# Optimization experiments

Hardware: AMD Instinct MI355X
Metric: run time of the kernel (lower is better)

The kernel has to match this reference:

```python
import math
import jax, jax.numpy as jnp
import numpy as np

SHAPES = [(80, 80), (40, 40), (20, 20), (10, 10)]
BS, LQ, D, NH, NL, NP = 8, 1000, 256, 8, 4, 4
C = D // NH


def _offset_bias():
    # replicates _reset_parameters grid_init bias for sampling_offsets
    thetas = np.arange(NH, dtype=np.float32) * (2.0 * math.pi / NH)
    grid = np.stack([np.cos(thetas), np.sin(thetas)], -1)  # [NH,2]
    grid = grid / np.abs(grid).max(-1, keepdims=True)
    grid = np.tile(grid[:, None, None, :], (1, NL, NP, 1))  # [NH,NL,NP,2]
    for i in range(NP):
        grid[:, :, i, :] *= i + 1
    return jnp.asarray(grid.reshape(-1))


def setup_inputs() -> dict:
    key = jax.random.key(0)
    ks = jax.random.split(key, 8)
    len_v = sum(h * w for h, w in SHAPES)
    s = 1.0 / math.sqrt(D)
    starts = np.cumsum([0] + [h * w for h, w in SHAPES])[:-1]
    return {
        "query": jax.random.normal(ks[0], (BS, LQ, D), jnp.float32),
        "reference_points": jax.random.uniform(ks[1], (BS, LQ, NL, 2), jnp.float32),
        "value": jax.random.normal(ks[2], (BS, len_v, D), jnp.float32),
        "w_off": jax.random.normal(ks[3], (D, NH * NL * NP * 2), jnp.float32) * 0.01,
        "b_off": _offset_bias(),
        "w_attn": jax.random.normal(ks[4], (D, NH * NL * NP), jnp.float32) * 0.01,
        "b_attn": jnp.zeros((NH * NL * NP,), jnp.float32),
        "w_v": jax.random.normal(ks[5], (D, D), jnp.float32) * s,
        "b_v": jnp.zeros((D,), jnp.float32),
        "w_o": jax.random.normal(ks[6], (D, D), jnp.float32) * s,
        "b_o": jnp.zeros((D,), jnp.float32),
        "value_spatial_shapes": jnp.array(SHAPES, jnp.int32),
        "value_level_start_index": jnp.array(starts, jnp.int32),
    }


def _sample(img, grid, H, W):
    # bilinear grid_sample, padding_mode='zeros', align_corners=False
    # img: [B, C, H*W], grid: [B, Q, P, 2] in [-1, 1] -> out [B, C, Q, P]
    x = (grid[..., 0] + 1.0) * (W * 0.5) - 0.5
    y = (grid[..., 1] + 1.0) * (H * 0.5) - 0.5
    x0 = jnp.floor(x)
    y0 = jnp.floor(y)
    fx = x - x0
    fy = y - y0
    x0i = x0.astype(jnp.int32)
    y0i = y0.astype(jnp.int32)

    def gather(xi, yi, w):
        valid = (xi >= 0) & (xi < W) & (yi >= 0) & (yi < H)
        idx = jnp.clip(yi, 0, H - 1) * W + jnp.clip(xi, 0, W - 1)
        B, Q, P = idx.shape
        g = jax.vmap(lambda im, ix: im[:, ix])(img, idx.reshape(B, Q * P))  # [B,C,QP]
        return g.reshape(B, -1, Q, P) * (w * valid)[:, None]

    return (gather(x0i, y0i, (1 - fx) * (1 - fy))
            + gather(x0i + 1, y0i, fx * (1 - fy))
            + gather(x0i, y0i + 1, (1 - fx) * fy)
            + gather(x0i + 1, y0i + 1, fx * fy))


def _forward(query, reference_points, value, w_off, b_off, w_attn, b_attn,
             w_v, b_v, w_o, b_o, shapes):
    bs, lq, _ = query.shape
    v = (value @ w_v + b_v).reshape(bs, -1, NH, C)  # [bs, len_v, NH, C]
    off = (query @ w_off + b_off).reshape(bs, lq, NH, NL, NP, 2)
    attn = jax.nn.softmax((query @ w_attn + b_attn).reshape(bs, lq, NH, NL * NP), axis=-1)
    attn = attn.reshape(bs, lq, NH, NL, NP)
    # offset normalizer is spatial_shapes flipped -> (W, H) per level
    norm = jnp.array([[w, h] for h, w in shapes], dtype=query.dtype)  # [NL,2]
    loc = reference_points[:, :, None, :, None, :] + off / norm[None, None, None, :, None, :]
    grids = 2.0 * loc - 1.0  # [bs,lq,NH,NL,NP,2]
    start = 0
    sampled = []
    for lvl, (H, W) in enumerate(shapes):
        v_l = v[:, start:start + H * W].transpose(0, 2, 3, 1).reshape(bs * NH, C, H * W)
        g_l = grids[:, :, :, lvl].transpose(0, 2, 1, 3, 4).reshape(bs * NH, lq, NP, 2)
        sampled.append(_sample(v_l, g_l, H, W))  # [bs*NH, C, lq, NP]
        start += H * W
    samp = jnp.stack(sampled, axis=3).reshape(bs * NH, C, lq, NL * NP)
    aw = attn.transpose(0, 2, 1, 3, 4).reshape(bs * NH, 1, lq, NL * NP)
    out = (samp * aw).sum(-1).reshape(bs, NH * C, lq).transpose(0, 2, 1)  # [bs,lq,D]
    return out @ w_o + b_o


def reference(query, reference_points, value, w_off, b_off, w_attn, b_attn,
              w_v, b_v, w_o, b_o, value_spatial_shapes, value_level_start_index):
    shapes = [tuple(int(x) for x in r) for r in np.asarray(value_spatial_shapes)]
    return _forward(query, reference_points, value, w_off, b_off, w_attn, b_attn,
                    w_v, b_v, w_o, b_o, shapes)
```

## Files before the change

kernel.cpp:

```cpp
#include <hip/hip_runtime.h>
#include <hip/hip_bf16.h>
#include <math.h>

#define BS     8
#define LQ     1000
#define DMODEL 256
#define NH     8
#define NLV    4
#define NPT    4
#define LEN_V  8500
#define NQ     (BS*LQ)
#define MV     (BS*LEN_V)
#define KS     8

typedef __attribute__((ext_vector_type(8))) short short8;
typedef __attribute__((ext_vector_type(4))) float floatx4;

static __device__ __forceinline__ unsigned short f2bf(float f) {
    __hip_bfloat16 h = __float2bfloat16(f);
    return __builtin_bit_cast(unsigned short, h);
}
static __device__ __forceinline__ float asf(unsigned int u) {
    return __builtin_bit_cast(float, u);
}

template <bool A_BF16, bool OUT_BF16>
__global__ __launch_bounds__(256, 2) void mfma_gemm_db(
    const void* __restrict__ Aptr, const unsigned short* __restrict__ Bfrag,
    const float* __restrict__ bias1, const float* __restrict__ bias2, int nsplit,
    void* __restrict__ Cptr, int M)
{
    __shared__ unsigned short As[2][16384];

    const int tid = threadIdx.x;
    const int l   = tid & 63;
    const int w   = tid >> 6;
    const int bn  = blockIdx.y;
    const int lm  = l & 15;
    const int lk  = l >> 4;
    const int x7  = lm & 7;
    const int N   = (int)gridDim.y * 128;
    const int n_mtiles = (M + 63) >> 6;

    short8 Bf[2][KS];
    const int u0 = bn * 8 + w * 2;
    #pragma unroll
    for (int j = 0; j < 2; ++j)
        #pragma unroll
        for (int s = 0; s < KS; ++s)
            Bf[j][s] = *(const short8*)(Bfrag + ((size_t)((u0 + j) * KS + s) * 64 + l) * 8);

    const unsigned short* Ab = (const unsigned short*)Aptr;
    const float*          Af = (const float*)Aptr;

    float4 holdf[16];
    short8 holdb[8];

    auto prefetch = [&](int tile) {
        if (A_BF16) {
            #pragma unroll
            for (int j = 0; j < 8; ++j) {
                const int vi  = j * 256 + tid;
                const int row = vi >> 5, g = vi & 31;
                int grow = tile * 64 + row; grow = grow < M ? grow : M - 1;
                holdb[j] = *(const short8*)(Ab + (size_t)grow * 256 + g * 8);
            }
        } else {
            #pragma unroll
            for (int j = 0; j < 16; ++j) {
                const int vi  = j * 256 + tid;
                const int row = vi >> 6, c4 = vi & 63;
                int grow = tile * 64 + row; grow = grow < M ? grow : M - 1;
                holdf[j] = *(const float4*)(Af + (size_t)grow * 256 + c4 * 4);
            }
        }
    };

    int bm  = blockIdx.x;
    int buf = 0;
    prefetch(bm);

    while (bm < n_mtiles) {
        const int bm_next = bm + (int)gridDim.x;

        if (A_BF16) {
            #pragma unroll
            for (int j = 0; j < 8; ++j) {
                const int vi  = j * 256 + tid;
                const int row = vi >> 5, g = vi & 31;
                const int phys = g ^ (row & 7);
                *(short8*)(&As[buf][row * 256 + phys * 8]) = holdb[j];
            }
        } else {
            #pragma unroll
            for (int j = 0; j < 16; ++j) {
                const int vi  = j * 256 + tid;
                const int row = vi >> 6, c4 = vi & 63;
                const int g = c4 >> 1, half = c4 & 1;
                const int phys = g ^ (row & 7);
                float4 f = holdf[j];
                ushort4 h;
                h.x = f2bf(f.x); h.y = f2bf(f.y); h.z = f2bf(f.z); h.w = f2bf(f.w);
                *(ushort4*)(&As[buf][row * 256 + phys * 8 + half * 4]) = h;
            }
        }
        __syncthreads();

        if (bm_next < n_mtiles) prefetch(bm_next);

        floatx4 acc[4][2];
        #pragma unroll
        for (int i = 0; i < 4; ++i)
            #pragma unroll
            for (int j = 0; j < 2; ++j)
                #pragma unroll
                for (int r = 0; r < 4; ++r) acc[i][j][r] = 0.f;

        #pragma unroll
        for (int s = 0; s < KS; ++s) {
            short8 afr[4];
            #pragma unroll
            for (int i = 0; i < 4; ++i)
                afr[i] = *(const short8*)(
                    &As[buf][(i * 16 + lm) * 256 + (((s * 4 + lk) ^ x7)) * 8]);
            #pragma unroll
            for (int i = 0; i < 4; ++i)
                #pragma unroll
                for (int j = 0; j < 2; ++j)
                    acc[i][j] = __builtin_amdgcn_mfma_f32_16x16x32_bf16(
                                    afr[i], Bf[j][s], acc[i][j], 0, 0, 0);
        }

        #pragma unroll
        for (int j = 0; j < 2; ++j) {
            const int col = bn * 128 + w * 32 + j * 16 + lm;
            const float bv = (bias2 != nullptr && col >= nsplit) ? bias2[col - nsplit]
                                                                 : bias1[col];
            #pragma unroll
            for (int i = 0; i < 4; ++i) {
                const int rbase = bm * 64 + i * 16 + lk * 4;
                #pragma unroll
                for (int r = 0; r < 4; ++r) {
                    const int row = rbase + r;
                    if (row < M) {
                        const float v = acc[i][j][r] + bv;
                        if (OUT_BF16)
                            ((unsigned short*)Cptr)[(size_t)row * N + col] = f2bf(v);
                        else
                            ((float*)Cptr)[(size_t)row * N + col] = v;
                    }
                }
            }
        }

        buf ^= 1;
        bm = bm_next;
    }
}

__global__ __launch_bounds__(256) void wtransform(
    const float* __restrict__ w_v, const float* __restrict__ w_off,
    const float* __restrict__ w_attn, const float* __restrict__ w_o,
    unsigned short* __restrict__ wv_f, unsigned short* __restrict__ woa_f,
    unsigned short* __restrict__ wo_f)
{
    const int gid = blockIdx.x * 256 + threadIdx.x;
    int chunk, mode;
    if (gid < 8192)               { chunk = gid;         mode = 0; }
    else if (gid < 8192 + 12288)  { chunk = gid - 8192;  mode = 1; }
    else                          { chunk = gid - 20480; mode = 2; }
    const int l = chunk & 63, s = (chunk >> 6) & 7, u = chunk >> 9;
    short8 o;
    #pragma unroll
    for (int j = 0; j < 8; ++j) {
        const int k = s * 32 + (l >> 4) * 8 + j;
        const int n = u * 16 + (l & 15);
        float v;
        if (mode == 0)      v = w_v[k * 256 + n];
        else if (mode == 1) v = (n < 256) ? w_off[k * 256 + n] : w_attn[k * 128 + (n - 256)];
        else                v = w_o[k * 256 + n];
        o[j] = (short)f2bf(v);
    }
    unsigned short* dp = (mode == 0 ? wv_f : mode == 1 ? woa_f : wo_f)
                         + ((size_t)(u * 8 + s) * 64 + l) * 8;
    *(short8*)dp = o;
}

__global__ __launch_bounds__(256) void ms_sample(
    const unsigned short* __restrict__ v,
    const float* __restrict__ offattn,
    const float* __restrict__ refp,
    unsigned short* __restrict__ out_pre)
{
    __shared__ float offx_s[8][16][8];
    __shared__ float offy_s[8][16][8];
    __shared__ float atw_s [8][16][8];
    __shared__ float ref_s [8][8];

    const int tid = threadIdx.x;
    const int iq0 = blockIdx.x * 8;

    if (tid < 64) {
        const int q = tid >> 3, h = tid & 7;
        const float* rowp = offattn + (size_t)(iq0 + q) * 384;
        float lg[16];
        float m = -1e30f;
        #pragma unroll
        for (int i = 0; i < 16; ++i) { lg[i] = rowp[256 + h * 16 + i]; m = fmaxf(m, lg[i]); }
        float s = 0.f;
        #pragma unroll
        for (int i = 0; i < 16; ++i) { lg[i] = __expf(lg[i] - m); s += lg[i]; }
        const float inv = 1.f / s;
        #pragma unroll
        for (int i = 0; i < 16; ++i) atw_s[q][i][h] = lg[i] * inv;
        #pragma unroll
        for (int i = 0; i < 16; ++i) {
            offx_s[q][i][h] = rowp[(h * 16 + i) * 2 + 0];
            offy_s[q][i][h] = rowp[(h * 16 + i) * 2 + 1];
        }
        if (h == 0) {
            #pragma unroll
            for (int i = 0; i < 8; ++i) ref_s[q][i] = refp[(size_t)(iq0 + q) * 8 + i];
        }
    }
    __syncthreads();

    const int q8  = tid >> 5;
    const int sub = tid & 31;
    const int h   = sub >> 2;
    const int oct = sub & 3;
    const int iq  = iq0 + q8;
    const int b   = iq / LQ;

    float acc[8] = {0.f, 0.f, 0.f, 0.f, 0.f, 0.f, 0.f, 0.f};
    const unsigned short* vb = v + (size_t)b * LEN_V * 256 + h * 32 + oct * 8;
    const int Hs[4] = {80, 40, 20, 10};
    const int st[4] = {0, 6400, 8000, 8400};

    #pragma unroll
    for (int lvl = 0; lvl < NLV; ++lvl) {
        const int W = Hs[lvl];
        const float bx = ref_s[q8][lvl * 2 + 0] * (float)W - 0.5f;
        const float by = ref_s[q8][lvl * 2 + 1] * (float)W - 0.5f;
        const unsigned short* vl = vb + (size_t)st[lvl] * 256;
        #pragma unroll
        for (int p = 0; p < NPT; ++p) {
            const int lp = lvl * 4 + p;
            const float x  = bx + offx_s[q8][lp][h];
            const float y  = by + offy_s[q8][lp][h];
            const float at = atw_s[q8][lp][h];
            const float x0f = floorf(x), y0f = floorf(y);
            const float fx = x - x0f, fy = y - y0f;
            const int x0 = (int)x0f, y0 = (int)y0f;
            const int x1 = x0 + 1,   y1 = y0 + 1;
            const int cx0 = min(max(x0, 0), W - 1);
            const int cx1 = min(max(x1, 0), W - 1);
            const int cy0 = min(max(y0, 0), W - 1);
            const int cy1 = min(max(y1, 0), W - 1);
            const float vx0 = (x0 >= 0 && x0 < W) ? 1.f : 0.f;
            const float vx1 = (x1 >= 0 && x1 < W) ? 1.f : 0.f;
            const float vy0 = (y0 >= 0 && y0 < W) ? 1.f : 0.f;
            const float vy1 = (y1 >= 0 && y1 < W) ? 1.f : 0.f;
            const float w00 = at * (1.f - fx) * (1.f - fy) * vx0 * vy0;
            const float w01 = at * fx * (1.f - fy) * vx1 * vy0;
            const float w10 = at * (1.f - fx) * fy * vx0 * vy1;
            const float w11 = at * fx * fy * vx1 * vy1;
            const unsigned short* r0 = vl + (size_t)(cy0 * W) * 256;
            const unsigned short* r1 = vl + (size_t)(cy1 * W) * 256;
            const uint4 d00 = *(const uint4*)(r0 + (size_t)cx0 * 256);
            const uint4 d01 = *(const uint4*)(r0 + (size_t)cx1 * 256);
            const uint4 d10 = *(const uint4*)(r1 + (size_t)cx0 * 256);
            const uint4 d11 = *(const uint4*)(r1 + (size_t)cx1 * 256);
            acc[0] += w00 * asf(d00.x << 16) + w01 * asf(d01.x << 16)
                    + w10 * asf(d10.x << 16) + w11 * asf(d11.x << 16);
            acc[1] += w00 * asf(d00.x & 0xffff0000u) + w01 * asf(d01.x & 0xffff0000u)
                    + w10 * asf(d10.x & 0xffff0000u) + w11 * asf(d11.x & 0xffff0000u);
            acc[2] += w00 * asf(d00.y << 16) + w01 * asf(d01.y << 16)
                    + w10 * asf(d10.y << 16) + w11 * asf(d11.y << 16);
            acc[3] += w00 * asf(d00.y & 0xffff0000u) + w01 * asf(d01.y & 0xffff0000u)
                    + w10 * asf(d10.y & 0xffff0000u) + w11 * asf(d11.y & 0xffff0000u);
            acc[4] += w00 * asf(d00.z << 16) + w01 * asf(d01.z << 16)
                    + w10 * asf(d10.z << 16) + w11 * asf(d11.z << 16);
            acc[5] += w00 * asf(d00.z & 0xffff0000u) + w01 * asf(d01.z & 0xffff0000u)
                    + w10 * asf(d10.z & 0xffff0000u) + w11 * asf(d11.z & 0xffff0000u);
            acc[6] += w00 * asf(d00.w << 16) + w01 * asf(d01.w << 16)
                    + w10 * asf(d10.w << 16) + w11 * asf(d11.w << 16);
            acc[7] += w00 * asf(d00.w & 0xffff0000u) + w01 * asf(d01.w & 0xffff0000u)
                    + w10 * asf(d10.w & 0xffff0000u) + w11 * asf(d11.w & 0xffff0000u);
        }
    }

    short8 o;
    #pragma unroll
    for (int j = 0; j < 8; ++j) o[j] = (short)f2bf(acc[j]);
    *(short8*)(out_pre + (size_t)iq * 256 + sub * 8) = o;
}

extern "C" void kernel_launch(void* const* d_in, const int* in_sizes, int n_in,
                              void* d_out, int out_size, void* d_ws, size_t ws_size,
                              hipStream_t stream)
{
    const float* query  = (const float*)d_in[0];
    const float* refp   = (const float*)d_in[1];
    const float* value  = (const float*)d_in[2];
    const float* w_off  = (const float*)d_in[3];
    const float* b_off  = (const float*)d_in[4];
    const float* w_attn = (const float*)d_in[5];
    const float* b_attn = (const float*)d_in[6];
    const float* w_v    = (const float*)d_in[7];
    const float* b_v    = (const float*)d_in[8];
    const float* w_o    = (const float*)d_in[9];
    const float* b_o    = (const float*)d_in[10];
    (void)d_in[11]; (void)d_in[12];

    float* out = (float*)d_out;

    char* ws = (char*)d_ws;
    unsigned short* v_proj  = (unsigned short*)ws;
    float*          offattn = (float*)(ws + 34816000);
    unsigned short* outpre  = (unsigned short*)(ws + 47104000);
    unsigned short* wv_f    = (unsigned short*)(ws + 51200000);
    unsigned short* woa_f   = (unsigned short*)(ws + 51331072);
    unsigned short* wo_f    = (unsigned short*)(ws + 51527680);

    dim3 blk(256);

    hipLaunchKernelGGL(wtransform, dim3(112), blk, 0, stream,
                       w_v, w_off, w_attn, w_o, wv_f, woa_f, wo_f);
    hipLaunchKernelGGL((mfma_gemm_db<false, true>), dim3(256, 2), blk, 0, stream,
                       value, wv_f, b_v, nullptr, 1 << 30, v_proj, MV);
    hipLaunchKernelGGL((mfma_gemm_db<false, false>), dim3(63, 3), blk, 0, stream,
                       query, woa_f, b_off, b_attn, 256, offattn, NQ);
    hipLaunchKernelGGL(ms_sample, dim3(1000), blk, 0, stream,
                       v_proj, offattn, refp, outpre);
    hipLaunchKernelGGL((mfma_gemm_db<true, false>), dim3(63, 2), blk, 0, stream,
                       outpre, wo_f, b_o, nullptr, 1 << 30, out, NQ);
}
```

Measured before the change: 214.3 us.

## Pre-cast inputs to bf16, DMA-load GEMM tiles, fuse output projection into sampler

```diff
diff --git a/kernel.cpp b/kernel.cpp
--- a/kernel.cpp
+++ b/kernel.cpp
@@ -24,9 +24,16 @@
     return __builtin_bit_cast(float, u);
 }
 
-template <bool A_BF16, bool OUT_BF16>
-__global__ __launch_bounds__(256, 2) void mfma_gemm_db(
-    const void* __restrict__ Aptr, const unsigned short* __restrict__ Bfrag,
+static __device__ __forceinline__ void dma16(const unsigned short* g, unsigned short* lds) {
+    __builtin_amdgcn_global_load_lds(
+        (const __attribute__((address_space(1))) unsigned int*)g,
+        (__attribute__((address_space(3))) unsigned int*)lds,
+        16, 0, 0);
+}
+
+template <bool OUT_BF16>
+__global__ __launch_bounds__(256, 2) void mfma_gemm_dma(
+    const unsigned short* __restrict__ Ab, const unsigned short* __restrict__ Bfrag,
     const float* __restrict__ bias1, const float* __restrict__ bias2, int nsplit,
     void* __restrict__ Cptr, int M)
 {
@@ -50,63 +57,29 @@
         for (int s = 0; s < KS; ++s)
             Bf[j][s] = *(const short8*)(Bfrag + ((size_t)((u0 + j) * KS + s) * 64 + l) * 8);
 
-    const unsigned short* Ab = (const unsigned short*)Aptr;
-    const float*          Af = (const float*)Aptr;
-
-    float4 holdf[16];
-    short8 holdb[8];
-
-    auto prefetch = [&](int tile) {
-        if (A_BF16) {
-            #pragma unroll
-            for (int j = 0; j < 8; ++j) {
-                const int vi  = j * 256 + tid;
-                const int row = vi >> 5, g = vi & 31;
-                int grow = tile * 64 + row; grow = grow < M ? grow : M - 1;
-                holdb[j] = *(const short8*)(Ab + (size_t)grow * 256 + g * 8);
-            }
-        } else {
-            #pragma unroll
-            for (int j = 0; j < 16; ++j) {
-                const int vi  = j * 256 + tid;
-                const int row = vi >> 6, c4 = vi & 63;
-                int grow = tile * 64 + row; grow = grow < M ? grow : M - 1;
-                holdf[j] = *(const float4*)(Af + (size_t)grow * 256 + c4 * 4);
-            }
+    auto dma_tile = [&](int tile, int buf) {
+        #pragma unroll
+        for (int j = 0; j < 8; ++j) {
+            const int slot = j * 256 + tid;
+            const int row  = slot >> 5;
+            const int gp   = slot & 31;
+            const int gc   = gp ^ (row & 7);
+            int grow = tile * 64 + row; grow = grow < M ? grow : M - 1;
+            dma16(Ab + (size_t)grow * 256 + gc * 8,
+                  &As[buf][(j * 256 + w * 64) * 8]);
         }
     };
 
     int bm  = blockIdx.x;
     int buf = 0;
-    prefetch(bm);
+    if (bm < n_mtiles) dma_tile(bm, 0);
 
     while (bm < n_mtiles) {
         const int bm_next = bm + (int)gridDim.x;
 
-        if (A_BF16) {
-            #pragma unroll
-            for (int j = 0; j < 8; ++j) {
-                const int vi  = j * 256 + tid;
-                const int row = vi >> 5, g = vi & 31;
-                const int phys = g ^ (row & 7);
-                *(short8*)(&As[buf][row * 256 + phys * 8]) = holdb[j];
-            }
-        } else {
-            #pragma unroll
-            for (int j = 0; j < 16; ++j) {
-                const int vi  = j * 256 + tid;
-                const int row = vi >> 6, c4 = vi & 63;
-                const int g = c4 >> 1, half = c4 & 1;
-                const int phys = g ^ (row & 7);
-                float4 f = holdf[j];
-                ushort4 h;
-                h.x = f2bf(f.x); h.y = f2bf(f.y); h.z = f2bf(f.z); h.w = f2bf(f.w);
-                *(ushort4*)(&As[buf][row * 256 + phys * 8 + half * 4]) = h;
-            }
-        }
+        __builtin_amdgcn_s_waitcnt(0);
         __syncthreads();
-
-        if (bm_next < n_mtiles) prefetch(bm_next);
+        if (bm_next < n_mtiles) dma_tile(bm_next, buf ^ 1);
 
         floatx4 acc[4][2];
         #pragma unroll
@@ -186,19 +159,35 @@
     *(short8*)dp = o;
 }
 
-__global__ __launch_bounds__(256) void ms_sample(
+__global__ __launch_bounds__(256) void cast2_bf16(const float* __restrict__ value,
+                                                  const float* __restrict__ query,
+                                                  unsigned short* __restrict__ out)
+{
+    const int i = blockIdx.x * 256 + threadIdx.x;
+    const float4 v = (i < 4352000) ? ((const float4*)value)[i]
+                                   : ((const float4*)query)[i - 4352000];
+    ushort4 o;
+    o.x = f2bf(v.x); o.y = f2bf(v.y); o.z = f2bf(v.z); o.w = f2bf(v.w);
+    ((ushort4*)out)[i] = o;
+}
+
+__global__ __launch_bounds__(256) void ms_sample_fused(
     const unsigned short* __restrict__ v,
     const float* __restrict__ offattn,
     const float* __restrict__ refp,
-    unsigned short* __restrict__ out_pre)
+    const unsigned short* __restrict__ wo_f,
+    const float* __restrict__ b_o,
+    float* __restrict__ out)
 {
     __shared__ float offx_s[8][16][8];
     __shared__ float offy_s[8][16][8];
     __shared__ float atw_s [8][16][8];
     __shared__ float ref_s [8][8];
+    __shared__ unsigned short P[8][256];
 
     const int tid = threadIdx.x;
-    const int iq0 = blockIdx.x * 8;
+    const int bswz = blockIdx.x & 7;
+    const int iq0  = bswz * 1000 + (blockIdx.x >> 3) * 8;
 
     if (tid < 64) {
         const int q = tid >> 3, h = tid & 7;
@@ -229,11 +218,9 @@
     const int sub = tid & 31;
     const int h   = sub >> 2;
     const int oct = sub & 3;
-    const int iq  = iq0 + q8;
-    const int b   = iq / LQ;
 
     float acc[8] = {0.f, 0.f, 0.f, 0.f, 0.f, 0.f, 0.f, 0.f};
-    const unsigned short* vb = v + (size_t)b * LEN_V * 256 + h * 32 + oct * 8;
+    const unsigned short* vb = v + (size_t)bswz * LEN_V * 256 + h * 32 + oct * 8;
     const int Hs[4] = {80, 40, 20, 10};
     const int st[4] = {0, 6400, 8000, 8400};
 
@@ -290,10 +277,50 @@
         }
     }
 
-    short8 o;
-    #pragma unroll
-    for (int j = 0; j < 8; ++j) o[j] = (short)f2bf(acc[j]);
-    *(short8*)(out_pre + (size_t)iq * 256 + sub * 8) = o;
+    {
+        short8 o;
+        #pragma unroll
+        for (int j = 0; j < 8; ++j) o[j] = (short)f2bf(acc[j]);
+        *(short8*)(&P[q8][sub * 8]) = o;
+    }
+    __syncthreads();
+
+    const int l  = tid & 63;
+    const int w  = tid >> 6;
+    const int lm = l & 15;
+    const int lk = l >> 4;
+
+    floatx4 acc2[4];
+    #pragma unroll
+    for (int jj = 0; jj < 4; ++jj)
+        #pragma unroll
+        for (int r = 0; r < 4; ++r) acc2[jj][r] = 0.f;
+
+    #pragma unroll
+    for (int s = 0; s < KS; ++s) {
+        short8 afr;
+        if (lm < 8) afr = *(const short8*)(&P[lm][s * 32 + lk * 8]);
+        else { short8 z = {0,0,0,0,0,0,0,0}; afr = z; }
+        #pragma unroll
+        for (int jj = 0; jj < 4; ++jj) {
+            const int u = w * 4 + jj;
+            short8 bfr = *(const short8*)(wo_f + ((size_t)(u * KS + s) * 64 + l) * 8);
+            acc2[jj] = __builtin_amdgcn_mfma_f32_16x16x32_bf16(afr, bfr, acc2[jj], 0, 0, 0);
+        }
+    }
+
+    if (lk < 2) {
+        #pragma unroll
+        for (int jj = 0; jj < 4; ++jj) {
+            const int col = w * 64 + jj * 16 + lm;
+            const float bv = b_o[col];
+            #pragma unroll
+            for (int r = 0; r < 4; ++r) {
+                const int row = lk * 4 + r;
+                out[(size_t)(iq0 + row) * 256 + col] = acc2[jj][r] + bv;
+            }
+        }
+    }
 }
 
 extern "C" void kernel_launch(void* const* d_in, const int* in_sizes, int n_in,
@@ -316,23 +343,23 @@
     float* out = (float*)d_out;
 
     char* ws = (char*)d_ws;
-    unsigned short* v_proj  = (unsigned short*)ws;
-    float*          offattn = (float*)(ws + 34816000);
-    unsigned short* outpre  = (unsigned short*)(ws + 47104000);
-    unsigned short* wv_f    = (unsigned short*)(ws + 51200000);
-    unsigned short* woa_f   = (unsigned short*)(ws + 51331072);
-    unsigned short* wo_f    = (unsigned short*)(ws + 51527680);
+    unsigned short* valq_bf = (unsigned short*)ws;
+    unsigned short* v_proj  = (unsigned short*)(ws + 38912000);
+    float*          offattn = (float*)(ws + 73728000);
+    unsigned short* wv_f    = (unsigned short*)(ws + 86016000);
+    unsigned short* woa_f   = (unsigned short*)(ws + 86147072);
+    unsigned short* wo_f    = (unsigned short*)(ws + 86343680);
 
     dim3 blk(256);
 
     hipLaunchKernelGGL(wtransform, dim3(112), blk, 0, stream,
                        w_v, w_off, w_attn, w_o, wv_f, woa_f, wo_f);
-    hipLaunchKernelGGL((mfma_gemm_db<false, true>), dim3(256, 2), blk, 0, stream,
-                       value, wv_f, b_v, nullptr, 1 << 30, v_proj, MV);
-    hipLaunchKernelGGL((mfma_gemm_db<false, false>), dim3(63, 3), blk, 0, stream,
-                       query, woa_f, b_off, b_attn, 256, offattn, NQ);
-    hipLaunchKernelGGL(ms_sample, dim3(1000), blk, 0, stream,
-                       v_proj, offattn, refp, outpre);
-    hipLaunchKernelGGL((mfma_gemm_db<true, false>), dim3(63, 2), blk, 0, stream,
-                       outpre, wo_f, b_o, nullptr, 1 << 30, out, NQ);
-}
+    hipLaunchKernelGGL(cast2_bf16, dim3(19000), blk, 0, stream,
+                       value, query, valq_bf);
+    hipLaunchKernelGGL((mfma_gemm_dma<true>), dim3(532, 2), blk, 0, stream,
+                       valq_bf, wv_f, b_v, nullptr, 1 << 30, v_proj, MV);
+    hipLaunchKernelGGL((mfma_gemm_dma<false>), dim3(125, 3), blk, 0, stream,
+                       valq_bf + (size_t)MV * 256, woa_f, b_off, b_attn, 256, offattn, NQ);
+    hipLaunchKernelGGL(ms_sample_fused, dim3(1000), blk, 0, stream,
+                       v_proj, offattn, refp, wo_f, b_o, out);
+}
```

Measured after the change: 213.2 us. Within noise of the previous version (-0.5%).
